# Kernel tuning notes

Hardware: AMD Instinct MI355X
Metric: run time of the kernel (lower is better)

The kernel has to match this reference:

```python
import jax, jax.numpy as jnp
import numpy as np

B, T, D, F, E, K = 4, 2048, 1024, 2048, 8, 2


def setup_inputs() -> dict:
    key = jax.random.key(0)
    ks = jax.random.split(key, 5)
    s = lambda n: 1.0 / np.sqrt(n)
    return {
        "x": jax.random.normal(ks[0], (B, T, D), jnp.float32),
        "gate_w": jax.random.normal(ks[1], (D, E), jnp.float32) * s(D),
        "gate_b": jnp.zeros((E,), jnp.float32),
        "w1": jax.random.normal(ks[2], (E, D, F), jnp.float32) * s(D),
        "b1": jnp.zeros((E, F), jnp.float32),
        "w2": jax.random.normal(ks[3], (E, F, D), jnp.float32) * s(F),
        "b2": jnp.zeros((E, D), jnp.float32),
    }


def reference(x, gate_w, gate_b, w1, b1, w2, b2):
    # Router: gate logits -> top-k -> softmax over the k selected logits
    logits = x @ gate_w + gate_b                      # [B,T,E]
    top_v, top_i = jax.lax.top_k(logits, K)           # [B,T,K]
    top_w = jax.nn.softmax(top_v, axis=-1)            # [B,T,K]
    # Dense combine weights per expert: w_full[b,t,e] = sum_k top_w * 1[top_i==e]
    one_hot = jax.nn.one_hot(top_i, E, dtype=x.dtype)  # [B,T,K,E]
    w_full = jnp.sum(top_w[..., None] * one_hot, axis=-2)  # [B,T,E]
    # All-experts FFN (batched over expert dim), exact-erf GELU as in nn.GELU()
    h = jax.nn.gelu(jnp.einsum('btd,edf->ebtf', x, w1) + b1[:, None, None, :],
                    approximate=False)                 # [E,B,T,F]
    y = jnp.einsum('ebtf,efd->ebtd', h, w2) + b2[:, None, None, :]  # [E,B,T,D]
    # Weighted combine (zero weight for unselected experts == masked dispatch)
    return jnp.einsum('bte,ebtd->btd', w_full, y)      # [B,T,D]
```

## Files before the change

kernel.cpp:

```cpp
#include <hip/hip_runtime.h>
#include <hip/hip_bf16.h>
#include <math.h>

#define B_ 4
#define T_ 2048
#define D_ 1024
#define F_ 2048
#define E_ 8
#define NT (B_ * T_)
#define NS (NT * 2)
#define CAP (NS + E_ * 128)

typedef __attribute__((ext_vector_type(8))) short short8;
typedef __attribute__((ext_vector_type(4))) float floatx4;

static __device__ __forceinline__ unsigned short f2bf(float f) {
  union { float f; unsigned u; } a; a.f = f;
  unsigned r = a.u + 0x7fffu + ((a.u >> 16) & 1u);
  return (unsigned short)(r >> 16);
}

static __device__ __forceinline__ float bf2f(unsigned u) {
  union { unsigned u; float f; } a; a.u = u << 16; return a.f;
}

static __device__ __forceinline__ void gld16(const unsigned short* g, unsigned short* l) {
  __builtin_amdgcn_global_load_lds(
      (const __attribute__((address_space(1))) void*)g,
      (__attribute__((address_space(3))) void*)l, 16, 0, 0);
}

static __device__ __forceinline__ float gelu_f(float v) {
  float ax = fabsf(v) * 0.70710678118654752f;
  float t = __builtin_amdgcn_rcpf(1.f + 0.3275911f * ax);
  float e = __builtin_amdgcn_exp2f(-ax * ax * 1.44269504088896f);
  float p = t * (0.254829592f +
            t * (-0.284496736f +
            t * (1.421413741f +
            t * (-1.453152027f +
            t * 1.061405429f))));
  float er = 1.f - p * e;
  er = copysignf(er, v);
  return 0.5f * v * (1.f + er);
}

__global__ void transpose_cvt(const float* __restrict__ in, unsigned short* __restrict__ out,
                              int R, int C) {
  __shared__ float tile[64][65];
  int e = blockIdx.z;
  const float* inp = in + (size_t)e * R * C;
  unsigned short* outp = out + (size_t)e * R * C;
  int c0 = blockIdx.x * 64, r0 = blockIdx.y * 64;
  int tid = threadIdx.x;
  int rl = tid >> 4;
  int cl = (tid & 15) * 4;
#pragma unroll
  for (int jr = 0; jr < 4; jr++) {
    int row = rl + 16 * jr;
    float4 v = *(const float4*)&inp[(size_t)(r0 + row) * C + c0 + cl];
    tile[row][cl + 0] = v.x; tile[row][cl + 1] = v.y;
    tile[row][cl + 2] = v.z; tile[row][cl + 3] = v.w;
  }
  __syncthreads();
  int cc0 = tid >> 3;
  int rq = (tid & 7) * 8;
#pragma unroll
  for (int jc = 0; jc < 2; jc++) {
    int cc = cc0 + 32 * jc;
    unsigned w[4];
#pragma unroll
    for (int i = 0; i < 4; i++) {
      unsigned lo = f2bf(tile[rq + 2 * i][cc]);
      unsigned hi = f2bf(tile[rq + 2 * i + 1][cc]);
      w[i] = lo | (hi << 16);
    }
    *(uint4*)&outp[(size_t)(c0 + cc) * R + r0 + rq] = make_uint4(w[0], w[1], w[2], w[3]);
  }
}

__global__ void router_k(const float* __restrict__ x, const float* __restrict__ gw,
                         const float* __restrict__ gb, int* __restrict__ ti,
                         float* __restrict__ tw) {
  int wid = threadIdx.x >> 6, lane = threadIdx.x & 63;
  int t = blockIdx.x * 4 + wid;
  const float* xr = x + (size_t)t * D_;
  float acc[E_];
#pragma unroll
  for (int e = 0; e < E_; e++) acc[e] = 0.f;
#pragma unroll
  for (int it = 0; it < D_ / 64; it++) {
    int d = it * 64 + lane;
    float xv = xr[d];
    const float* g = gw + d * E_;
#pragma unroll
    for (int e = 0; e < E_; e++) acc[e] += xv * g[e];
  }
#pragma unroll
  for (int off = 32; off > 0; off >>= 1)
#pragma unroll
    for (int e = 0; e < E_; e++) acc[e] += __shfl_xor(acc[e], off);
  if (lane == 0) {
    float v[E_];
#pragma unroll
    for (int e = 0; e < E_; e++) v[e] = acc[e] + gb[e];
    int i0 = 0; float v0 = v[0];
#pragma unroll
    for (int e = 1; e < E_; e++) if (v[e] > v0) { v0 = v[e]; i0 = e; }
    int i1 = -1; float v1 = -3.4e38f;
#pragma unroll
    for (int e = 0; e < E_; e++) if (e != i0 && v[e] > v1) { v1 = v[e]; i1 = e; }
    float ex = expf(v1 - v0);
    float w0 = 1.f / (1.f + ex);
    float w1 = ex / (1.f + ex);
    ti[2 * t] = i0; tw[2 * t] = w0;
    ti[2 * t + 1] = i1; tw[2 * t + 1] = w1;
  }
}

__global__ void count_prefix_k(const int* __restrict__ ti, int* __restrict__ offs,
                               int* __restrict__ cursors) {
  __shared__ int scnt[4][E_];
  int tid = threadIdx.x;
  int cnt[E_];
#pragma unroll
  for (int k = 0; k < E_; k++) cnt[k] = 0;
  for (int i = tid; i < NS; i += 256) {
    int e = ti[i];
#pragma unroll
    for (int k = 0; k < E_; k++) cnt[k] += (e == k) ? 1 : 0;
  }
#pragma unroll
  for (int off = 32; off > 0; off >>= 1)
#pragma unroll
    for (int k = 0; k < E_; k++) cnt[k] += __shfl_xor(cnt[k], off);
  int wid = tid >> 6, lane = tid & 63;
  if (lane == 0)
#pragma unroll
    for (int k = 0; k < E_; k++) scnt[wid][k] = cnt[k];
  __syncthreads();
  if (tid == 0) {
    int o = 0;
    for (int k = 0; k < E_; k++) {
      int c = scnt[0][k] + scnt[1][k] + scnt[2][k] + scnt[3][k];
      offs[k] = o;
      cursors[k] = o;
      o += (c + 127) & ~127;
    }
    offs[E_] = o;
  }
}

__global__ void scatter_k(const int* __restrict__ ti, const float* __restrict__ tw,
                          int* __restrict__ cursors, int* __restrict__ idx,
                          int* __restrict__ pos_of) {
  int a = blockIdx.x * 256 + threadIdx.x;
  int lane = threadIdx.x & 63;
  int e = ti[a];
  unsigned long long m[E_];
#pragma unroll
  for (int k = 0; k < E_; k++) m[k] = __ballot(e == k);
  int base = 0;
  if (lane < E_) base = atomicAdd(&cursors[lane], __popcll(m[lane]));
  int myBase = __shfl(base, e);
  unsigned long long m_mine = 0;
#pragma unroll
  for (int k = 0; k < E_; k++) if (e == k) m_mine = m[k];
  int rank = __popcll(m_mine & ((1ull << lane) - 1ull));
  int pos = myBase + rank;
  idx[pos] = a >> 1;
  pos_of[a] = pos;
}

__global__ void gather_k(const float* __restrict__ x, const int* __restrict__ idx,
                         unsigned short* __restrict__ Xg) {
  int s = blockIdx.x;
  int t = idx[s];
  t = ((unsigned)t < (unsigned)NT) ? t : 0;
  const float4* xr = (const float4*)(x + (size_t)t * D_);
  float4 v = xr[threadIdx.x];
  uint2 p;
  p.x = (unsigned)f2bf(v.x) | ((unsigned)f2bf(v.y) << 16);
  p.y = (unsigned)f2bf(v.z) | ((unsigned)f2bf(v.w) << 16);
  ((uint2*)(Xg + (size_t)s * D_))[threadIdx.x] = p;
}

template <int K, int N, bool GELU>
__global__ __launch_bounds__(256, 3) void gemm_k(const unsigned short* __restrict__ A,
                                                 const unsigned short* __restrict__ W,
                                                 const float* __restrict__ bias_all,
                                                 unsigned short* __restrict__ O,
                                                 const int* __restrict__ offs) {
  constexpr int NC = N / 128;
  int h = blockIdx.x;
  int logical = (h & 7) * ((int)gridDim.x >> 3) + (h >> 3);
  int rt = logical / NC, ct = logical - rt * NC;
  int slot0 = rt * 128;
  if (slot0 >= offs[E_]) return;
  int e = 0;
  while (slot0 >= offs[e + 1]) e++;
  const unsigned short* Bp = W + (size_t)e * N * K;
  int n0 = ct * 128;

  __shared__ unsigned short lA[3][128 * 32];
  __shared__ unsigned short lB[3][128 * 32];

  int tid = threadIdx.x;
  int wid = tid >> 6, lane = tid & 63;
  int wr = wid >> 1, wc = wid & 1;
  int quad = lane >> 4, l15 = lane & 15;

  int cph = (((l15 & 1) << 2) | quad) ^ ((l15 >> 1) & 7);
  int ra = ((wr << 5) + (l15 >> 1)) * 64 + cph * 8;
  int rb = ((wc << 5) + (l15 >> 1)) * 64 + cph * 8;

  int srl = lane >> 3;
  int clog = (lane & 7) ^ srl;
  int r_l = (srl << 1) | (clog >> 2);
  int q_l = clog & 3;
  const unsigned short* gA = A + (size_t)(slot0 + 32 * wid + r_l) * K + q_l * 8;
  const unsigned short* gB = Bp + (size_t)(n0 + 32 * wid + r_l) * K + q_l * 8;

#define STG(buf, kt) do {                                                \
    gld16(gA + (size_t)(kt) * 32, &lA[buf][(32 * wid) * 32]);            \
    gld16(gA + (size_t)16 * K + (size_t)(kt) * 32,                       \
          &lA[buf][(32 * wid + 16) * 32]);                               \
    gld16(gB + (size_t)(kt) * 32, &lB[buf][(32 * wid) * 32]);            \
    gld16(gB + (size_t)16 * K + (size_t)(kt) * 32,                       \
          &lB[buf][(32 * wid + 16) * 32]);                               \
  } while (0)
#define SYNC4 asm volatile("s_waitcnt vmcnt(4)\n\ts_barrier" ::: "memory")

  floatx4 acc[4][4];
#pragma unroll
  for (int mi = 0; mi < 4; mi++)
#pragma unroll
    for (int ni = 0; ni < 4; ni++) acc[mi][ni] = (floatx4){0.f, 0.f, 0.f, 0.f};

  constexpr int NK = K / 32;

  STG(0, 0);
  STG(1, 1);
  SYNC4;

#define STEP(j, t) do {                                                  \
    int kt = ((t) + 2 < NK) ? (t) + 2 : 0;                               \
    STG(((j) + 2) % 3, kt);                                              \
    short8 af[4], bfr[4];                                                \
    _Pragma("unroll")                                                    \
    for (int m = 0; m < 4; m++) af[m] = *(const short8*)&lA[j][ra + m * 512]; \
    _Pragma("unroll")                                                    \
    for (int n = 0; n < 4; n++) bfr[n] = *(const short8*)&lB[j][rb + n * 512]; \
    _Pragma("unroll")                                                    \
    for (int m = 0; m < 4; m++)                                          \
      _Pragma("unroll")                                                  \
      for (int n = 0; n < 4; n++)                                        \
        acc[m][n] = __builtin_amdgcn_mfma_f32_16x16x32_bf16(af[m], bfr[n], acc[m][n], 0, 0, 0); \
    SYNC4;                                                               \
  } while (0)

  for (int t3 = 0; t3 < NK; t3 += 3) {
    STEP(0, t3);
    if (t3 + 1 < NK) STEP(1, t3 + 1);
    if (t3 + 2 < NK) STEP(2, t3 + 2);
  }
#undef STEP
#undef STG
#undef SYNC4

  const float* bias = bias_all + (size_t)e * N;
#pragma unroll
  for (int mi = 0; mi < 4; mi++) {
    int row = slot0 + 64 * wr + 16 * mi + quad * 4;
#pragma unroll
    for (int ni = 0; ni < 4; ni++) {
      int col = n0 + 64 * wc + 16 * ni + l15;
      float bv = bias[col];
#pragma unroll
      for (int r = 0; r < 4; r++) {
        float v = acc[mi][ni][r] + bv;
        if (GELU) v = gelu_f(v);
        O[(size_t)(row + r) * N + col] = f2bf(v);
      }
    }
  }
}

__global__ void combine_k(const unsigned short* __restrict__ Yg,
                          const int* __restrict__ pos_of,
                          const float* __restrict__ tw, float* __restrict__ out) {
  int t = blockIdx.x;
  int p0 = pos_of[2 * t], p1 = pos_of[2 * t + 1];
  float w0 = tw[2 * t], w1 = tw[2 * t + 1];
  uint2 a = ((const uint2*)(Yg + (size_t)p0 * D_))[threadIdx.x];
  uint2 b = ((const uint2*)(Yg + (size_t)p1 * D_))[threadIdx.x];
  float4 r;
  r.x = w0 * bf2f(a.x & 0xffffu) + w1 * bf2f(b.x & 0xffffu);
  r.y = w0 * bf2f(a.x >> 16)     + w1 * bf2f(b.x >> 16);
  r.z = w0 * bf2f(a.y & 0xffffu) + w1 * bf2f(b.y & 0xffffu);
  r.w = w0 * bf2f(a.y >> 16)     + w1 * bf2f(b.y >> 16);
  ((float4*)(out + (size_t)t * D_))[threadIdx.x] = r;
}

extern "C" void kernel_launch(void* const* d_in, const int* in_sizes, int n_in,
                              void* d_out, int out_size, void* d_ws, size_t ws_size,
                              hipStream_t stream) {
  const float* x  = (const float*)d_in[0];
  const float* gw = (const float*)d_in[1];
  const float* gb = (const float*)d_in[2];
  const float* w1 = (const float*)d_in[3];
  const float* b1 = (const float*)d_in[4];
  const float* w2 = (const float*)d_in[5];
  const float* b2 = (const float*)d_in[6];
  float* out = (float*)d_out;

  char* p = (char*)d_ws;
  unsigned short* w1t = (unsigned short*)p; p += (size_t)E_ * D_ * F_ * 2;
  unsigned short* w2t = (unsigned short*)p; p += (size_t)E_ * D_ * F_ * 2;
  unsigned short* Xg  = (unsigned short*)p; p += (size_t)CAP * D_ * 2;
  unsigned short* H   = (unsigned short*)p; p += (size_t)CAP * F_ * 2;
  int*   idx    = (int*)p; p += (size_t)CAP * 4;
  int*   pos_of = (int*)p; p += (size_t)NS * 4;
  int*   ti     = (int*)p; p += (size_t)NS * 4;
  float* tw     = (float*)p; p += (size_t)NS * 4;
  int* cursors = (int*)p; p += 64;
  int* offs    = (int*)p; p += 64;
  unsigned short* Yg = Xg;

  transpose_cvt<<<dim3(F_ / 64, D_ / 64, E_), 256, 0, stream>>>(w1, w1t, D_, F_);
  transpose_cvt<<<dim3(D_ / 64, F_ / 64, E_), 256, 0, stream>>>(w2, w2t, F_, D_);
  router_k<<<NT / 4, 256, 0, stream>>>(x, gw, gb, ti, tw);
  count_prefix_k<<<1, 256, 0, stream>>>(ti, offs, cursors);
  scatter_k<<<NS / 256, 256, 0, stream>>>(ti, tw, cursors, idx, pos_of);
  gather_k<<<CAP, 256, 0, stream>>>(x, idx, Xg);
  gemm_k<D_, F_, true><<<dim3((CAP / 128) * (F_ / 128)), 256, 0, stream>>>(Xg, w1t, b1, H, offs);
  gemm_k<F_, D_, false><<<dim3((CAP / 128) * (D_ / 128)), 256, 0, stream>>>(H, w2t, b2, Yg, offs);
  combine_k<<<NT, 256, 0, stream>>>(Yg, pos_of, tw, out);
}
```

Baseline: 465.0 us.

## Fuse combine into second GEMM via atomics, merge transposes, double-buffer GEMM

```diff
diff --git a/kernel.cpp b/kernel.cpp
--- a/kernel.cpp
+++ b/kernel.cpp
@@ -44,13 +44,18 @@
   return 0.5f * v * (1.f + er);
 }
 
-__global__ void transpose_cvt(const float* __restrict__ in, unsigned short* __restrict__ out,
-                              int R, int C) {
+__global__ void transpose_cvt(const float* __restrict__ w1, const float* __restrict__ w2,
+                              unsigned short* __restrict__ w1t, unsigned short* __restrict__ w2t) {
   __shared__ float tile[64][65];
-  int e = blockIdx.z;
-  const float* inp = in + (size_t)e * R * C;
-  unsigned short* outp = out + (size_t)e * R * C;
-  int c0 = blockIdx.x * 64, r0 = blockIdx.y * 64;
+  int id = blockIdx.x;
+  bool second = id >= 512;
+  int lid = second ? id - 512 : id;
+  int R = second ? F_ : D_, C = second ? D_ : F_;
+  int nx = C / 64;
+  int ty = lid / nx, tx = lid - ty * nx;
+  const float* inp = (second ? w2 : w1) + (size_t)blockIdx.y * R * C;
+  unsigned short* outp = (second ? w2t : w1t) + (size_t)blockIdx.y * R * C;
+  int c0 = tx * 64, r0 = ty * 64;
   int tid = threadIdx.x;
   int rl = tid >> 4;
   int cl = (tid & 15) * 4;
@@ -80,7 +85,15 @@
 
 __global__ void router_k(const float* __restrict__ x, const float* __restrict__ gw,
                          const float* __restrict__ gb, int* __restrict__ ti,
-                         float* __restrict__ tw) {
+                         float* __restrict__ tw, float* __restrict__ out,
+                         float* __restrict__ wt_of) {
+  int gtid = blockIdx.x * 256 + threadIdx.x;
+  float4 z = {0.f, 0.f, 0.f, 0.f};
+  float4* ob = (float4*)out;
+#pragma unroll
+  for (int j = 0; j < 4; j++) ob[gtid + j * (NT * D_ / 16)] = z;
+  if (gtid < CAP) wt_of[gtid] = 0.f;
+
   int wid = threadIdx.x >> 6, lane = threadIdx.x & 63;
   int t = blockIdx.x * 4 + wid;
   const float* xr = x + (size_t)t * D_;
@@ -152,7 +165,7 @@
 
 __global__ void scatter_k(const int* __restrict__ ti, const float* __restrict__ tw,
                           int* __restrict__ cursors, int* __restrict__ idx,
-                          int* __restrict__ pos_of) {
+                          float* __restrict__ wt_of) {
   int a = blockIdx.x * 256 + threadIdx.x;
   int lane = threadIdx.x & 63;
   int e = ti[a];
@@ -168,7 +181,7 @@
   int rank = __popcll(m_mine & ((1ull << lane) - 1ull));
   int pos = myBase + rank;
   idx[pos] = a >> 1;
-  pos_of[a] = pos;
+  wt_of[pos] = tw[a];
 }
 
 __global__ void gather_k(const float* __restrict__ x, const int* __restrict__ idx,
@@ -184,12 +197,15 @@
   ((uint2*)(Xg + (size_t)s * D_))[threadIdx.x] = p;
 }
 
-template <int K, int N, bool GELU>
-__global__ __launch_bounds__(256, 3) void gemm_k(const unsigned short* __restrict__ A,
+template <int K, int N, bool GELU, bool ATOMIC>
+__global__ __launch_bounds__(256, 5) void gemm_k(const unsigned short* __restrict__ A,
                                                  const unsigned short* __restrict__ W,
                                                  const float* __restrict__ bias_all,
                                                  unsigned short* __restrict__ O,
-                                                 const int* __restrict__ offs) {
+                                                 const int* __restrict__ offs,
+                                                 const int* __restrict__ idxp,
+                                                 const float* __restrict__ wtp,
+                                                 float* __restrict__ outp) {
   constexpr int NC = N / 128;
   int h = blockIdx.x;
   int logical = (h & 7) * ((int)gridDim.x >> 3) + (h >> 3);
@@ -201,8 +217,8 @@
   const unsigned short* Bp = W + (size_t)e * N * K;
   int n0 = ct * 128;
 
-  __shared__ unsigned short lA[3][128 * 32];
-  __shared__ unsigned short lB[3][128 * 32];
+  __shared__ unsigned short lA[2][128 * 32];
+  __shared__ unsigned short lB[2][128 * 32];
 
   int tid = threadIdx.x;
   int wid = tid >> 6, lane = tid & 63;
@@ -228,7 +244,7 @@
     gld16(gB + (size_t)16 * K + (size_t)(kt) * 32,                       \
           &lB[buf][(32 * wid + 16) * 32]);                               \
   } while (0)
-#define SYNC4 asm volatile("s_waitcnt vmcnt(4)\n\ts_barrier" ::: "memory")
+#define SYNC0 asm volatile("s_waitcnt vmcnt(0)\n\ts_barrier" ::: "memory")
 
   floatx4 acc[4][4];
 #pragma unroll
@@ -239,66 +255,68 @@
   constexpr int NK = K / 32;
 
   STG(0, 0);
-  STG(1, 1);
-  SYNC4;
-
-#define STEP(j, t) do {                                                  \
-    int kt = ((t) + 2 < NK) ? (t) + 2 : 0;                               \
-    STG(((j) + 2) % 3, kt);                                              \
+  SYNC0;
+
+#define STEP(bufc, t) do {                                               \
+    int kt = ((t) + 1 < NK) ? (t) + 1 : 0;   \
+    STG((bufc) ^ 1, kt);                                                 \
     short8 af[4], bfr[4];                                                \
     _Pragma("unroll")                                                    \
-    for (int m = 0; m < 4; m++) af[m] = *(const short8*)&lA[j][ra + m * 512]; \
+    for (int m = 0; m < 4; m++) af[m] = *(const short8*)&lA[bufc][ra + m * 512]; \
     _Pragma("unroll")                                                    \
-    for (int n = 0; n < 4; n++) bfr[n] = *(const short8*)&lB[j][rb + n * 512]; \
+    for (int n = 0; n < 4; n++) bfr[n] = *(const short8*)&lB[bufc][rb + n * 512]; \
     _Pragma("unroll")                                                    \
     for (int m = 0; m < 4; m++)                                          \
       _Pragma("unroll")                                                  \
       for (int n = 0; n < 4; n++)                                        \
         acc[m][n] = __builtin_amdgcn_mfma_f32_16x16x32_bf16(af[m], bfr[n], acc[m][n], 0, 0, 0); \
-    SYNC4;                                                               \
+    SYNC0;                                                               \
   } while (0)
 
-  for (int t3 = 0; t3 < NK; t3 += 3) {
-    STEP(0, t3);
-    if (t3 + 1 < NK) STEP(1, t3 + 1);
-    if (t3 + 2 < NK) STEP(2, t3 + 2);
+  for (int t2 = 0; t2 < NK; t2 += 2) {
+    STEP(0, t2);
+    STEP(1, t2 + 1);
   }
 #undef STEP
 #undef STG
-#undef SYNC4
+#undef SYNC0
 
   const float* bias = bias_all + (size_t)e * N;
-#pragma unroll
-  for (int mi = 0; mi < 4; mi++) {
-    int row = slot0 + 64 * wr + 16 * mi + quad * 4;
-#pragma unroll
-    for (int ni = 0; ni < 4; ni++) {
-      int col = n0 + 64 * wc + 16 * ni + l15;
-      float bv = bias[col];
+  if constexpr (ATOMIC) {
+#pragma unroll
+    for (int mi = 0; mi < 4; mi++) {
+      int srow = slot0 + 64 * wr + 16 * mi + quad * 4;
 #pragma unroll
       for (int r = 0; r < 4; r++) {
-        float v = acc[mi][ni][r] + bv;
-        if (GELU) v = gelu_f(v);
-        O[(size_t)(row + r) * N + col] = f2bf(v);
+        int slot = srow + r;
+        int tok = idxp[slot];
+        tok = ((unsigned)tok < (unsigned)NT) ? tok : 0;
+        float w = wtp[slot];
+        float* orow = outp + (size_t)tok * D_;
+#pragma unroll
+        for (int ni = 0; ni < 4; ni++) {
+          int col = n0 + 64 * wc + 16 * ni + l15;
+          atomicAdd(&orow[col], w * (acc[mi][ni][r] + bias[col]));
+        }
       }
     }
-  }
-}
-
-__global__ void combine_k(const unsigned short* __restrict__ Yg,
-                          const int* __restrict__ pos_of,
-                          const float* __restrict__ tw, float* __restrict__ out) {
-  int t = blockIdx.x;
-  int p0 = pos_of[2 * t], p1 = pos_of[2 * t + 1];
-  float w0 = tw[2 * t], w1 = tw[2 * t + 1];
-  uint2 a = ((const uint2*)(Yg + (size_t)p0 * D_))[threadIdx.x];
-  uint2 b = ((const uint2*)(Yg + (size_t)p1 * D_))[threadIdx.x];
-  float4 r;
-  r.x = w0 * bf2f(a.x & 0xffffu) + w1 * bf2f(b.x & 0xffffu);
-  r.y = w0 * bf2f(a.x >> 16)     + w1 * bf2f(b.x >> 16);
-  r.z = w0 * bf2f(a.y & 0xffffu) + w1 * bf2f(b.y & 0xffffu);
-  r.w = w0 * bf2f(a.y >> 16)     + w1 * bf2f(b.y >> 16);
-  ((float4*)(out + (size_t)t * D_))[threadIdx.x] = r;
+  } else {
+#pragma unroll
+    for (int mi = 0; mi < 4; mi++) {
+      int row = slot0 + 64 * wr + 16 * mi + quad * 4;
+#pragma unroll
+      for (int ni = 0; ni < 4; ni++) {
+        int col = n0 + 64 * wc + 16 * ni + l15;
+        float bv = bias[col];
+#pragma unroll
+        for (int r = 0; r < 4; r++) {
+          float v = acc[mi][ni][r] + bv;
+          if (GELU) v = gelu_f(v);
+          O[(size_t)(row + r) * N + col] = f2bf(v);
+        }
+      }
+    }
+  }
 }
 
 extern "C" void kernel_launch(void* const* d_in, const int* in_sizes, int n_in,
@@ -319,20 +337,19 @@
   unsigned short* Xg  = (unsigned short*)p; p += (size_t)CAP * D_ * 2;
   unsigned short* H   = (unsigned short*)p; p += (size_t)CAP * F_ * 2;
   int*   idx    = (int*)p; p += (size_t)CAP * 4;
-  int*   pos_of = (int*)p; p += (size_t)NS * 4;
+  float* wt_of  = (float*)p; p += (size_t)CAP * 4;
   int*   ti     = (int*)p; p += (size_t)NS * 4;
   float* tw     = (float*)p; p += (size_t)NS * 4;
   int* cursors = (int*)p; p += 64;
   int* offs    = (int*)p; p += 64;
-  unsigned short* Yg = Xg;
-
-  transpose_cvt<<<dim3(F_ / 64, D_ / 64, E_), 256, 0, stream>>>(w1, w1t, D_, F_);
-  transpose_cvt<<<dim3(D_ / 64, F_ / 64, E_), 256, 0, stream>>>(w2, w2t, F_, D_);
-  router_k<<<NT / 4, 256, 0, stream>>>(x, gw, gb, ti, tw);
+
+  transpose_cvt<<<dim3(1024, E_), 256, 0, stream>>>(w1, w2, w1t, w2t);
+  router_k<<<NT / 4, 256, 0, stream>>>(x, gw, gb, ti, tw, out, wt_of);
   count_prefix_k<<<1, 256, 0, stream>>>(ti, offs, cursors);
-  scatter_k<<<NS / 256, 256, 0, stream>>>(ti, tw, cursors, idx, pos_of);
+  scatter_k<<<NS / 256, 256, 0, stream>>>(ti, tw, cursors, idx, wt_of);
   gather_k<<<CAP, 256, 0, stream>>>(x, idx, Xg);
-  gemm_k<D_, F_, true><<<dim3((CAP / 128) * (F_ / 128)), 256, 0, stream>>>(Xg, w1t, b1, H, offs);
-  gemm_k<F_, D_, false><<<dim3((CAP / 128) * (D_ / 128)), 256, 0, stream>>>(H, w2t, b2, Yg, offs);
-  combine_k<<<NT, 256, 0, stream>>>(Yg, pos_of, tw, out);
-}
+  gemm_k<D_, F_, true, false><<<dim3((CAP / 128) * (F_ / 128)), 256, 0, stream>>>(
+      Xg, w1t, b1, H, offs, nullptr, nullptr, nullptr);
+  gemm_k<F_, D_, false, true><<<dim3((CAP / 128) * (D_ / 128)), 256, 0, stream>>>(
+      H, w2t, b2, nullptr, offs, idx, wt_of, out);
+}
```

Result: slower. 996.0 us (+114.2%).
